# Kernel optimization log

Measured on AMD Instinct MI355X. Metric: run time of the kernel, lower is better.

Reference implementation:

```python
import jax, jax.numpy as jnp
import numpy as np

BANDWIDTH = 0.1
N_STEPS = 5
TOL = 1e-3
BASE = 3
COORD_OFFSET = 512   # bins assumed within (-512, 511] per dim
COORD_BITS = 10      # 3 dims * 10 bits = 30 bits, fits int32


def _generate_offsets(d, base=3):
    # replicates torch.meshgrid(indexing='ij') over arange(-1, base-1)
    ranges = [np.arange(-1, base - 1) for _ in range(d)]
    mesh = np.meshgrid(*ranges, indexing='ij')
    return jnp.asarray(np.stack(mesh, axis=-1).reshape(-1, d), dtype=jnp.int32)


def _pack_keys(bins):
    # bins: (..., d) int32 -> unique scalar int32 key per bin coordinate
    d = bins.shape[-1]
    key = jnp.zeros(bins.shape[:-1], dtype=jnp.int32)
    for k in range(d):  # tiny fixed loop over dims
        key = (key << COORD_BITS) | (bins[..., k] + COORD_OFFSET)
    return key


def _step(X, offsets, bandwidth):
    # One mean-shift step: bin points, scatter-add sums/counts over the
    # union of offset-shifted bins (torch.unique replaced by exact key
    # packing + sort-based grouping, fixed shapes for jit).
    n, d = X.shape
    m = offsets.shape[0]  # base ** d
    bins = (X / bandwidth).astype(jnp.int32)          # trunc-toward-zero == torch .int()
    shifted = bins[:, None, :] + offsets[None, :, :]  # (n, m, d)
    keys = _pack_keys(shifted).reshape(-1)            # (n*m,)
    K = keys.shape[0]

    order = jnp.argsort(keys)
    skeys = keys[order]
    new_grp = jnp.concatenate(
        [jnp.zeros((1,), jnp.int32), (skeys[1:] != skeys[:-1]).astype(jnp.int32)]
    )
    seg = jnp.cumsum(new_grp)                         # group id per sorted position

    # X repeated once per offset (matches X.repeat(1, m).reshape(-1, d))
    Xflat = jnp.broadcast_to(X[:, None, :], (n, m, d)).reshape(-1, d)
    sum_per = jax.ops.segment_sum(Xflat[order], seg, num_segments=K)          # (K, d)
    cnt_per = jax.ops.segment_sum(jnp.ones((K,), X.dtype), seg, num_segments=K)

    # segment id per original (unsorted) flat position == inverse_indices
    seg_orig = jnp.zeros((K,), seg.dtype).at[order].set(seg)
    sum_mapped = sum_per[seg_orig].reshape(n, m, d).sum(axis=1)   # (n, d)
    cnt_mapped = cnt_per[seg_orig].reshape(n, m).sum(axis=1)      # (n,)
    return sum_mapped / cnt_mapped[:, None]


def setup_inputs() -> dict:
    key = jax.random.key(0)
    X = jax.random.normal(key, (200000, 3), dtype=jnp.float32)
    return {"X": X}


def reference(X):
    n, d = X.shape
    offsets = _generate_offsets(d, BASE)

    def body(carry, _):
        Xc, done = carry
        Xn = _step(Xc, offsets, BANDWIDTH)
        Xn = jnp.where(done, Xc, Xn)  # freeze once converged (== early break)
        conv = jnp.max(jnp.linalg.norm(Xn - Xc, axis=1)) <= TOL
        return (Xn, done | conv), None

    (Xout, _), _ = jax.lax.scan(body, (X, jnp.array(False)), None, length=N_STEPS)
    return Xout
```

## Files before the change

kernel.cpp:

```cpp
#include <hip/hip_runtime.h>


constexpr float BW   = 0.1f;
constexpr float TOL2 = 1e-6f;
constexpr int DIM  = 112, OFF = 56;
constexpr int DIM2 = DIM * DIM;
constexpr int CELLS = DIM * DIM * DIM;
constexpr int CLW = CELLS / 32;
constexpr int RDIM = 16, RC = 7;
constexpr int NREG = RDIM * RDIM * RDIM;
constexpr int RC3 = RC * RC * RC;
constexpr int NB_A = 128, BLK = 256;
constexpr int NF = 2048;
constexpr int IPB = 51;
constexpr float FPS = 16777216.0f;
constexpr double FPSI = 1.0 / 16777216.0;

typedef float vf2 __attribute__((ext_vector_type(2)));

__device__ __forceinline__ int clampb(int v) { return v < 0 ? 0 : (v > DIM - 1 ? DIM - 1 : v); }
__device__ __forceinline__ int binf(float v) { return clampb((int)(v / BW) + OFF); }
__device__ __forceinline__ int flatb(int bx, int by, int bz) { return (bx * DIM + by) * DIM + bz; }
__device__ __forceinline__ int regOf(int bx, int by, int bz) {
    return ((bx / RC) * RDIM + (by / RC)) * RDIM + (bz / RC);
}
__device__ __forceinline__ int lcOf(int bx, int by, int bz) {
    return ((bx % RC) * RC + (by % RC)) * RC + (bz % RC);
}

__device__ __forceinline__ void pk_add(float* p, float a, float b) {
#if defined(__has_builtin) && __has_builtin(__builtin_amdgcn_global_atomic_fadd_v2f32)
    vf2 v = {a, b};
    __builtin_amdgcn_global_atomic_fadd_v2f32((vf2*)p, v);
#else
    atomicAdd(p, a);
    atomicAdd(p + 1, b);
#endif
}

__launch_bounds__(BLK)
__global__ void k_histA(const float* __restrict__ X, int n, int* __restrict__ blockHist,
                        float4* __restrict__ zeroA, float4* __restrict__ zeroB) {
    __shared__ int h[NREG];
    for (int i = threadIdx.x; i < NREG; i += blockDim.x) h[i] = 0;
    __syncthreads();
    int stride = gridDim.x * blockDim.x;
    for (int i = blockIdx.x * blockDim.x + threadIdx.x; i < n; i += stride) {
        float x = X[3 * i + 0], y = X[3 * i + 1], z = X[3 * i + 2];
        atomicAdd(&h[regOf(binf(x), binf(y), binf(z))], 1);
    }
    __syncthreads();
    for (int i = threadIdx.x; i < NREG; i += blockDim.x)
        blockHist[blockIdx.x * NREG + i] = h[i];
    for (int i = blockIdx.x * blockDim.x + threadIdx.x; i < CELLS; i += stride) {
        zeroA[i] = make_float4(0.f, 0.f, 0.f, 0.f);
        zeroB[i] = make_float4(0.f, 0.f, 0.f, 0.f);
    }
}

__global__ void k_colscan(int* __restrict__ blockHist, int* __restrict__ regionPS) {
    int r = blockIdx.x * blockDim.x + threadIdx.x;
    if (r >= NREG) return;
    int run = 0;
    for (int b = 0; b < NB_A; ++b) {
        int idx = b * NREG + r;
        int v = blockHist[idx];
        blockHist[idx] = run;
        run += v;
    }
    regionPS[r] = run;
}

__launch_bounds__(1024)
__global__ void k_regprefix(int* __restrict__ regionPS) {
    __shared__ int buf[1024];
    int t = threadIdx.x;
    int v0 = regionPS[4 * t + 0], v1 = regionPS[4 * t + 1];
    int v2 = regionPS[4 * t + 2], v3 = regionPS[4 * t + 3];
    int s = v0 + v1 + v2 + v3;
    buf[t] = s;
    __syncthreads();
    for (int d = 1; d < 1024; d <<= 1) {
        int add = (t >= d) ? buf[t - d] : 0;
        __syncthreads();
        buf[t] += add;
        __syncthreads();
    }
    int excl = buf[t] - s;
    regionPS[4 * t + 0] = excl;
    regionPS[4 * t + 1] = excl + v0;
    regionPS[4 * t + 2] = excl + v0 + v1;
    regionPS[4 * t + 3] = excl + v0 + v1 + v2;
    if (t == 1023) regionPS[4096] = buf[1023];
}

__launch_bounds__(BLK)
__global__ void k_scatterA(const float* __restrict__ X, int n,
                           const int* __restrict__ blockHist,
                           const int* __restrict__ regionPS,
                           float4* __restrict__ bucket, float4* __restrict__ zeroC) {
    __shared__ int cur[NREG];
    for (int i = threadIdx.x; i < NREG; i += blockDim.x) cur[i] = 0;
    __syncthreads();
    int stride = gridDim.x * blockDim.x;
    for (int i = blockIdx.x * blockDim.x + threadIdx.x; i < n; i += stride) {
        float x = X[3 * i + 0], y = X[3 * i + 1], z = X[3 * i + 2];
        int r = regOf(binf(x), binf(y), binf(z));
        int pos = regionPS[r] + blockHist[blockIdx.x * NREG + r] + atomicAdd(&cur[r], 1);
        bucket[pos] = make_float4(x, y, z, __int_as_float(i));
    }
    for (int i = blockIdx.x * blockDim.x + threadIdx.x; i < CELLS; i += stride)
        zeroC[i] = make_float4(0.f, 0.f, 0.f, 0.f);
}

__launch_bounds__(BLK)
__global__ void k_binB(const float4* __restrict__ bucket, const int* __restrict__ regionPS,
                       float4* __restrict__ A, int* __restrict__ E0,
                       int* __restrict__ PIdx, int* __restrict__ gM0) {
    __shared__ unsigned long long aX[RC3], aY[RC3], aZ[RC3];
    __shared__ unsigned aC[RC3];
    __shared__ int cidx[RC3];
    __shared__ int cnt, cur, sBase;
    int r = blockIdx.x;
    for (int c = threadIdx.x; c < RC3; c += blockDim.x) {
        aX[c] = 0ull; aY[c] = 0ull; aZ[c] = 0ull; aC[c] = 0u;
    }
    if (threadIdx.x == 0) { cnt = 0; cur = 0; }
    __syncthreads();
    int start = regionPS[r], end = regionPS[r + 1];
    for (int i = start + threadIdx.x; i < end; i += blockDim.x) {
        float4 p = bucket[i];
        int lc = lcOf(binf(p.x), binf(p.y), binf(p.z));
        atomicAdd(&aX[lc], (unsigned long long)(long long)rintf(p.x * FPS));
        atomicAdd(&aY[lc], (unsigned long long)(long long)rintf(p.y * FPS));
        atomicAdd(&aZ[lc], (unsigned long long)(long long)rintf(p.z * FPS));
        atomicAdd(&aC[lc], 1u);
    }
    __syncthreads();
    int myc = 0;
    for (int c = threadIdx.x; c < RC3; c += blockDim.x)
        if (aC[c] > 0u) ++myc;
    if (myc) atomicAdd(&cnt, myc);
    __syncthreads();
    if (threadIdx.x == 0 && cnt > 0) sBase = atomicAdd(gM0, cnt);
    __syncthreads();
    int rx = r / (RDIM * RDIM), ry = (r / RDIM) % RDIM, rz = r % RDIM;
    for (int c = threadIdx.x; c < RC3; c += blockDim.x) {
        if (aC[c] > 0u) {
            int idx = sBase + atomicAdd(&cur, 1);
            cidx[c] = idx;
            int bx = rx * RC + c / (RC * RC);
            int by = ry * RC + (c / RC) % RC;
            int bz = rz * RC + c % RC;
            int b = flatb(bx, by, bz);
            E0[idx] = b;
            A[b] = make_float4((float)((double)(long long)aX[c] * FPSI),
                               (float)((double)(long long)aY[c] * FPSI),
                               (float)((double)(long long)aZ[c] * FPSI),
                               (float)aC[c]);
        }
    }
    __syncthreads();
    for (int i = start + threadIdx.x; i < end; i += blockDim.x) {
        float4 p = bucket[i];
        int lc = lcOf(binf(p.x), binf(p.y), binf(p.z));
        PIdx[__float_as_int(p.w)] = cidx[lc];
    }
}

__launch_bounds__(BLK)
__global__ void k_fused(
    const float4* __restrict__ src, const int* __restrict__ list, const int* __restrict__ pK,
    float4* __restrict__ REo, int* __restrict__ IDXo, float4* __restrict__ eposInit,
    float4* __restrict__ tgt, unsigned* __restrict__ clT,
    int updS, const float* __restrict__ X, int n, const int* __restrict__ PIdx,
    const float4* __restrict__ REp, const int* __restrict__ IDXp,
    const int* __restrict__ pM0, float4* __restrict__ epos,
    unsigned* __restrict__ notConv,
    const int* __restrict__ clearList, const int* __restrict__ pKc,
    float4* __restrict__ clearGrid, int chkMask, int lastStep) {
    __shared__ float4 sh[BLK];
    __shared__ float shW[IPB];
    __shared__ unsigned sFlag;
    if (threadIdx.x == 0) sFlag = 0;
    __syncthreads();
    int K = *pK;
    int NC = (K + IPB - 1) / IPB;
    int BC = NC;
    if (BC > NF - 256) BC = NF - 256;
    const float t5[5] = {1.f, 2.f, 3.f, 2.f, 1.f};
    bool moved = false;

    if ((int)blockIdx.x < BC) {
        bool frozen = false;
        if (chkMask) {
            #pragma unroll
            for (int t = 1; t <= 4; ++t)
                if ((chkMask >> t) & 1) frozen |= (notConv[t] == 0u);
        }
        if (!frozen) {
        int first, last, step;
        if (BC >= 64) {
            int xcd = blockIdx.x & 7, loc = blockIdx.x >> 3;
            int cpx = (NC + 7) >> 3;
            int bpx = ((BC - 1 - xcd) >> 3) + 1;
            first = xcd * cpx + loc;
            last = (xcd + 1) * cpx; if (last > NC) last = NC;
            step = bpx;
        } else {
            first = blockIdx.x; last = NC; step = BC;
        }
        for (int ib = first; ib < last; ib += step) {
            int li = threadIdx.x / 5;
            int dx = threadIdx.x % 5;
            int item = ib * IPB + li;
            float4 part = make_float4(0.f, 0.f, 0.f, 0.f);
            if (li < IPB && item < K) {
                int b = list[item];
                int bx = b / DIM2, rem = b % DIM2;
                int by = rem / DIM, bz = rem % DIM;
                if (dx == 2) shW[li] = src[b].w;
                int ix = bx + dx - 2;
                if ((unsigned)ix < (unsigned)DIM) {
                    float wx = t5[dx];
                    if (by >= 2 && by <= DIM - 3 && bz >= 2 && bz <= DIM - 3) {
                        const float4* bp = src + flatb(ix, by - 2, bz - 2);
                        float4 e0[5], e1[5];
                        #pragma unroll
                        for (int z = 0; z < 5; ++z) e0[z] = bp[z];
                        #pragma unroll
                        for (int z = 0; z < 5; ++z) e1[z] = bp[DIM + z];
                        #define ACC_ROW(EB, WXY)                                   \
                            {                                                      \
                                float wxy_ = (WXY);                                \
                                _Pragma("unroll")                                  \
                                for (int z = 0; z < 5; ++z) {                      \
                                    float w_ = wxy_ * t5[z];                       \
                                    part.x = fmaf(w_, EB[z].x, part.x);            \
                                    part.y = fmaf(w_, EB[z].y, part.y);            \
                                    part.z = fmaf(w_, EB[z].z, part.z);            \
                                    part.w = fmaf(w_, EB[z].w, part.w);            \
                                }                                                  \
                            }
                        ACC_ROW(e0, wx * 1.f);
                        #pragma unroll
                        for (int z = 0; z < 5; ++z) e0[z] = bp[2 * DIM + z];
                        ACC_ROW(e1, wx * 2.f);
                        #pragma unroll
                        for (int z = 0; z < 5; ++z) e1[z] = bp[3 * DIM + z];
                        ACC_ROW(e0, wx * 3.f);
                        #pragma unroll
                        for (int z = 0; z < 5; ++z) e0[z] = bp[4 * DIM + z];
                        ACC_ROW(e1, wx * 2.f);
                        ACC_ROW(e0, wx * 1.f);
                        #undef ACC_ROW
                    } else {
                        for (int dy = 0; dy < 5; ++dy) {
                            int iy = by + dy - 2;
                            if ((unsigned)iy >= (unsigned)DIM) continue;
                            float wxy = wx * t5[dy];
                            for (int dz = 0; dz < 5; ++dz) {
                                int iz = bz + dz - 2;
                                if ((unsigned)iz >= (unsigned)DIM) continue;
                                float w = wxy * t5[dz];
                                float4 e = src[flatb(ix, iy, iz)];
                                part.x = fmaf(w, e.x, part.x);
                                part.y = fmaf(w, e.y, part.y);
                                part.z = fmaf(w, e.z, part.z);
                                part.w = fmaf(w, e.w, part.w);
                            }
                        }
                    }
                }
            }
            sh[threadIdx.x] = part;
            __syncthreads();
            if (threadIdx.x < 64) {
                int item2 = ib * IPB + threadIdx.x;
                bool valid = (threadIdx.x < IPB) && (item2 < K);
                int bn = -1;
                float4 sv = make_float4(0.f, 0.f, 0.f, 0.f);
                if (valid) {
                    int base5 = threadIdx.x * 5;
                    float4 a0 = sh[base5 + 0], a1 = sh[base5 + 1], a2 = sh[base5 + 2];
                    float4 a3 = sh[base5 + 3], a4 = sh[base5 + 4];
                    float sx = a0.x + a1.x + a2.x + a3.x + a4.x;
                    float sy = a0.y + a1.y + a2.y + a3.y + a4.y;
                    float sz = a0.z + a1.z + a2.z + a3.z + a4.z;
                    float sc = a0.w + a1.w + a2.w + a3.w + a4.w;
                    int b = list[item2];
                    float W = shW[threadIdx.x];
                    float4 np = make_float4(sx / sc, sy / sc, sz / sc, W);
                    REo[item2] = np;
                    IDXo[b] = item2;
                    if (eposInit) eposInit[item2] = np;
                    if (!lastStep) {
                        bn = flatb(binf(np.x), binf(np.y), binf(np.z));
                        sv = make_float4(W * np.x, W * np.y, W * np.z, W);
                    }
                }
                if (!lastStep) {
                    int pbn = __shfl_up(bn, 1, 64);
                    unsigned f = (threadIdx.x == 0 || pbn != bn) ? 1u : 0u;
                    unsigned nf = __shfl_down(f, 1, 64);
                    bool leader = valid && (threadIdx.x == 63 || nf != 0u);
                    #pragma unroll
                    for (int off = 1; off < 64; off <<= 1) {
                        float ox = __shfl_up(sv.x, off, 64);
                        float oy = __shfl_up(sv.y, off, 64);
                        float oz = __shfl_up(sv.z, off, 64);
                        float ow = __shfl_up(sv.w, off, 64);
                        unsigned of = __shfl_up(f, off, 64);
                        if ((int)threadIdx.x >= off) {
                            if (!f) { sv.x += ox; sv.y += oy; sv.z += oz; sv.w += ow; }
                            f |= of;
                        }
                    }
                    if (leader) {
                        float* cell = (float*)&tgt[bn];
                        pk_add(cell + 0, sv.x, sv.y);
                        pk_add(cell + 2, sv.z, sv.w);
                        atomicOr(&clT[(unsigned)bn >> 5], 1u << (bn & 31));
                    }
                }
            }
            __syncthreads();
        }
        }
    } else {
        int U = (updS > 0) ? (X ? n : *pM0) : 0;
        int CL = clearList ? *pKc : 0;
        int total = U + CL;
        bool done = false;
        if (updS > 1) {
            for (int t = 1; t < updS; ++t) done |= (notConv[t] == 0u);
        }
        int stride = (NF - BC) * blockDim.x;
        for (int idx = (blockIdx.x - BC) * blockDim.x + threadIdx.x; idx < total;
             idx += stride) {
            if (idx < U) {
                int e = idx;
                if (X) {
                    float x = X[3 * e + 0], y = X[3 * e + 1], z = X[3 * e + 2];
                    float4 rr = REp[PIdx[e]];
                    float ex = rr.x - x, ey = rr.y - y, ez = rr.z - z;
                    moved |= (fmaf(ex, ex, fmaf(ey, ey, ez * ez)) > TOL2);
                } else if (!done) {
                    float4 p = epos[e];
                    int j = IDXp[flatb(binf(p.x), binf(p.y), binf(p.z))];
                    float4 rr = REp[j];
                    float ex = rr.x - p.x, ey = rr.y - p.y, ez = rr.z - p.z;
                    moved |= (fmaf(ex, ex, fmaf(ey, ey, ez * ez)) > TOL2);
                    epos[e] = make_float4(rr.x, rr.y, rr.z, p.w);
                }
            } else {
                clearGrid[clearList[idx - U]] = make_float4(0.f, 0.f, 0.f, 0.f);
            }
        }
    }
    if (moved) sFlag = 1;
    __syncthreads();
    if (threadIdx.x == 0 && updS > 0 && sFlag) notConv[updS] = 1u;
}

__launch_bounds__(BLK)
__global__ void k_compactM(unsigned* __restrict__ mask, int* __restrict__ listOut,
                           int* __restrict__ pKout) {
    __shared__ int scan[BLK];
    __shared__ int sBase;
    int i = blockIdx.x * blockDim.x + threadIdx.x;
    unsigned w = (i < CLW) ? mask[i] : 0u;
    if (i < CLW && w) mask[i] = 0u;
    int c = __popc(w);
    scan[threadIdx.x] = c;
    __syncthreads();
    for (int d = 1; d < BLK; d <<= 1) {
        int add = (threadIdx.x >= (unsigned)d) ? scan[threadIdx.x - d] : 0;
        __syncthreads();
        scan[threadIdx.x] += add;
        __syncthreads();
    }
    if (threadIdx.x == BLK - 1) {
        int tot = scan[BLK - 1];
        sBase = tot ? atomicAdd(pKout, tot) : 0;
    }
    __syncthreads();
    int base = sBase + scan[threadIdx.x] - c;
    int bb = i * 32;
    while (w) {
        int b = __ffs(w) - 1;
        listOut[base++] = bb + b;
        w &= w - 1;
    }
}

__global__ void k_map(const int* __restrict__ PIdx, int n, const float4* __restrict__ epos,
                      const float4* __restrict__ REa, const int* __restrict__ IDXa,
                      const unsigned* __restrict__ notConv, float* __restrict__ out) {
    bool done = false;
    for (int t = 1; t <= 4; ++t) done |= (notConv[t] == 0u);
    int i = blockIdx.x * blockDim.x + threadIdx.x;
    if (i >= n) return;
    float4 p = epos[PIdx[i]];
    if (!done) {
        float4 rr = REa[IDXa[flatb(binf(p.x), binf(p.y), binf(p.z))]];
        p.x = rr.x; p.y = rr.y; p.z = rr.z;
    }
    out[3 * i + 0] = p.x;
    out[3 * i + 1] = p.y;
    out[3 * i + 2] = p.z;
}

extern "C" void kernel_launch(void* const* d_in, const int* in_sizes, int n_in,
                              void* d_out, int out_size, void* d_ws, size_t ws_size,
                              hipStream_t stream) {
    const float* X = (const float*)d_in[0];
    int n = in_sizes[0] / 3;

    char* ws = (char*)d_ws;
    int*      cnt     = (int*)ws;
    unsigned* notConv = (unsigned*)(ws + 32);
    size_t mB = (size_t)CLW * 4;
    size_t gB = (size_t)CELLS * 16;
    unsigned* m0 = (unsigned*)(ws + 256);
    unsigned* m1 = (unsigned*)(ws + 256 + mB);
    float4* A = (float4*)(ws + 256 + 2 * mB);
    float4* B = (float4*)((char*)A + gB);
    float4* C = (float4*)((char*)B + gB);
    int* IDXa = (int*)((char*)C + gB);
    int* IDXb = IDXa + CELLS;
    float4* REa  = (float4*)(IDXb + CELLS);
    float4* REb  = REa + n;
    float4* epos = REb + n;
    int* E0   = (int*)(epos + n);
    int* La   = E0 + n;
    int* Lb   = La + n;
    int* Lc   = Lb + n;
    int* Ld   = Lc + n;
    int* PIdx = Ld + n;
    float4* bucket = (float4*)(PIdx + n);
    int* blockHist = (int*)(bucket + n);
    int* regionPS  = blockHist + NB_A * NREG;

    hipMemsetAsync(ws, 0, 256 + 2 * mB, stream);

    const int NCM = (CLW + BLK - 1) / BLK;

    k_histA<<<NB_A, BLK, 0, stream>>>(X, n, blockHist, A, B);
    k_colscan<<<NREG / BLK, BLK, 0, stream>>>(blockHist, regionPS);
    k_regprefix<<<1, 1024, 0, stream>>>(regionPS);
    k_scatterA<<<NB_A, BLK, 0, stream>>>(X, n, blockHist, regionPS, bucket, C);
    k_binB<<<NREG, BLK, 0, stream>>>(bucket, regionPS, A, E0, PIdx, &cnt[1]);

    k_fused<<<NF, BLK, 0, stream>>>(A, E0, &cnt[1], REa, IDXa, epos,
                                    B, m0,
                                    0, nullptr, n, nullptr, nullptr, nullptr, nullptr,
                                    nullptr, notConv, nullptr, nullptr, nullptr, 0, 0);
    k_compactM<<<NCM, BLK, 0, stream>>>(m0, La, &cnt[2]);
    k_fused<<<NF, BLK, 0, stream>>>(B, La, &cnt[2], REb, IDXb, nullptr,
                                    C, m1,
                                    1, X, n, PIdx, REa, IDXa, &cnt[1], nullptr,
                                    notConv, E0, &cnt[1], A, 0, 0);
    k_compactM<<<NCM, BLK, 0, stream>>>(m1, Lb, &cnt[3]);
    k_fused<<<NF, BLK, 0, stream>>>(C, Lb, &cnt[3], REa, IDXa, nullptr,
                                    A, m0,
                                    2, nullptr, n, nullptr, REb, IDXb, &cnt[1], epos,
                                    notConv, La, &cnt[2], B, 0b00010, 0);
    k_compactM<<<NCM, BLK, 0, stream>>>(m0, Lc, &cnt[4]);
    k_fused<<<NF, BLK, 0, stream>>>(A, Lc, &cnt[4], REb, IDXb, nullptr,
                                    B, m1,
                                    3, nullptr, n, nullptr, REa, IDXa, &cnt[1], epos,
                                    notConv, nullptr, nullptr, nullptr, 0b00110, 0);
    k_compactM<<<NCM, BLK, 0, stream>>>(m1, Ld, &cnt[5]);
    k_fused<<<NF, BLK, 0, stream>>>(B, Ld, &cnt[5], REa, IDXa, nullptr,
                                    nullptr, nullptr,
                                    4, nullptr, n, nullptr, REb, IDXb, &cnt[1], epos,
                                    notConv, nullptr, nullptr, nullptr, 0b01110, 1);

    k_map<<<(n + BLK - 1) / BLK, BLK, 0, stream>>>(PIdx, n, epos, REa, IDXa,
                                                   notConv, (float*)d_out);
}
```

Before: 246.6 us.

## Move per-point update and grid clearing from stencil kernel into compaction kernel

The stencil kernel previously split its blocks between grid-cell smoothing and auxiliary work: updating point positions, convergence checks and clearing the previous grid. That auxiliary work now runs in a new k_aux kernel that also does the mask compaction. The stencil kernel can therefore use all blocks for the cell work. The aux work now runs serially between stencil passes rather than alongside them, and the last stencil's frozen-check mask changes to include step 4.

```diff
diff --git a/kernel.cpp b/kernel.cpp
--- a/kernel.cpp
+++ b/kernel.cpp
@@ -13,6 +13,7 @@
 constexpr int NB_A = 128, BLK = 256;
 constexpr int NF = 2048;
 constexpr int IPB = 51;
+constexpr int NCM = (CLW + BLK - 1) / BLK;
 constexpr float FPS = 16777216.0f;
 constexpr double FPSI = 1.0 / 16777216.0;
 
@@ -173,161 +174,192 @@
     const float4* __restrict__ src, const int* __restrict__ list, const int* __restrict__ pK,
     float4* __restrict__ REo, int* __restrict__ IDXo, float4* __restrict__ eposInit,
     float4* __restrict__ tgt, unsigned* __restrict__ clT,
+    const unsigned* __restrict__ notConv, int chkMask, int lastStep) {
+    __shared__ float4 sh[BLK];
+    __shared__ float shW[IPB];
+    int K = *pK;
+    int NC = (K + IPB - 1) / IPB;
+    int BC = NC > NF ? NF : NC;
+    if ((int)blockIdx.x >= BC) return;
+    bool frozen = false;
+    if (chkMask) {
+        #pragma unroll
+        for (int t = 1; t <= 4; ++t)
+            if ((chkMask >> t) & 1) frozen |= (notConv[t] == 0u);
+    }
+    if (frozen) return;
+    const float t5[5] = {1.f, 2.f, 3.f, 2.f, 1.f};
+
+    int first, last, step;
+    if (BC >= 64) {
+        int xcd = blockIdx.x & 7, loc = blockIdx.x >> 3;
+        int cpx = (NC + 7) >> 3;
+        int bpx = ((BC - 1 - xcd) >> 3) + 1;
+        first = xcd * cpx + loc;
+        last = (xcd + 1) * cpx; if (last > NC) last = NC;
+        step = bpx;
+    } else {
+        first = blockIdx.x; last = NC; step = BC;
+    }
+    for (int ib = first; ib < last; ib += step) {
+        int li = threadIdx.x / 5;
+        int dx = threadIdx.x % 5;
+        int item = ib * IPB + li;
+        float4 part = make_float4(0.f, 0.f, 0.f, 0.f);
+        if (li < IPB && item < K) {
+            int b = list[item];
+            int bx = b / DIM2, rem = b % DIM2;
+            int by = rem / DIM, bz = rem % DIM;
+            if (dx == 2) shW[li] = src[b].w;
+            int ix = bx + dx - 2;
+            if ((unsigned)ix < (unsigned)DIM) {
+                float wx = t5[dx];
+                if (by >= 2 && by <= DIM - 3 && bz >= 2 && bz <= DIM - 3) {
+                    const float4* bp = src + flatb(ix, by - 2, bz - 2);
+                    float4 e0[5], e1[5];
+                    #pragma unroll
+                    for (int z = 0; z < 5; ++z) e0[z] = bp[z];
+                    #pragma unroll
+                    for (int z = 0; z < 5; ++z) e1[z] = bp[DIM + z];
+                    #define ACC_ROW(EB, WXY)                                   \
+                        {                                                      \
+                            float wxy_ = (WXY);                                \
+                            _Pragma("unroll")                                  \
+                            for (int z = 0; z < 5; ++z) {                      \
+                                float w_ = wxy_ * t5[z];                       \
+                                part.x = fmaf(w_, EB[z].x, part.x);            \
+                                part.y = fmaf(w_, EB[z].y, part.y);            \
+                                part.z = fmaf(w_, EB[z].z, part.z);            \
+                                part.w = fmaf(w_, EB[z].w, part.w);            \
+                            }                                                  \
+                        }
+                    ACC_ROW(e0, wx * 1.f);
+                    #pragma unroll
+                    for (int z = 0; z < 5; ++z) e0[z] = bp[2 * DIM + z];
+                    ACC_ROW(e1, wx * 2.f);
+                    #pragma unroll
+                    for (int z = 0; z < 5; ++z) e1[z] = bp[3 * DIM + z];
+                    ACC_ROW(e0, wx * 3.f);
+                    #pragma unroll
+                    for (int z = 0; z < 5; ++z) e0[z] = bp[4 * DIM + z];
+                    ACC_ROW(e1, wx * 2.f);
+                    ACC_ROW(e0, wx * 1.f);
+                    #undef ACC_ROW
+                } else {
+                    for (int dy = 0; dy < 5; ++dy) {
+                        int iy = by + dy - 2;
+                        if ((unsigned)iy >= (unsigned)DIM) continue;
+                        float wxy = wx * t5[dy];
+                        for (int dz = 0; dz < 5; ++dz) {
+                            int iz = bz + dz - 2;
+                            if ((unsigned)iz >= (unsigned)DIM) continue;
+                            float w = wxy * t5[dz];
+                            float4 e = src[flatb(ix, iy, iz)];
+                            part.x = fmaf(w, e.x, part.x);
+                            part.y = fmaf(w, e.y, part.y);
+                            part.z = fmaf(w, e.z, part.z);
+                            part.w = fmaf(w, e.w, part.w);
+                        }
+                    }
+                }
+            }
+        }
+        sh[threadIdx.x] = part;
+        __syncthreads();
+        if (threadIdx.x < 64) {
+            int item2 = ib * IPB + threadIdx.x;
+            bool valid = (threadIdx.x < IPB) && (item2 < K);
+            int bn = -1;
+            float4 sv = make_float4(0.f, 0.f, 0.f, 0.f);
+            if (valid) {
+                int base5 = threadIdx.x * 5;
+                float4 a0 = sh[base5 + 0], a1 = sh[base5 + 1], a2 = sh[base5 + 2];
+                float4 a3 = sh[base5 + 3], a4 = sh[base5 + 4];
+                float sx = a0.x + a1.x + a2.x + a3.x + a4.x;
+                float sy = a0.y + a1.y + a2.y + a3.y + a4.y;
+                float sz = a0.z + a1.z + a2.z + a3.z + a4.z;
+                float sc = a0.w + a1.w + a2.w + a3.w + a4.w;
+                int b = list[item2];
+                float W = shW[threadIdx.x];
+                float4 np = make_float4(sx / sc, sy / sc, sz / sc, W);
+                REo[item2] = np;
+                IDXo[b] = item2;
+                if (eposInit) eposInit[item2] = np;
+                if (!lastStep) {
+                    bn = flatb(binf(np.x), binf(np.y), binf(np.z));
+                    sv = make_float4(W * np.x, W * np.y, W * np.z, W);
+                }
+            }
+            if (!lastStep) {
+                int pbn = __shfl_up(bn, 1, 64);
+                unsigned f = (threadIdx.x == 0 || pbn != bn) ? 1u : 0u;
+                unsigned nf = __shfl_down(f, 1, 64);
+                bool leader = valid && (threadIdx.x == 63 || nf != 0u);
+                #pragma unroll
+                for (int off = 1; off < 64; off <<= 1) {
+                    float ox = __shfl_up(sv.x, off, 64);
+                    float oy = __shfl_up(sv.y, off, 64);
+                    float oz = __shfl_up(sv.z, off, 64);
+                    float ow = __shfl_up(sv.w, off, 64);
+                    unsigned of = __shfl_up(f, off, 64);
+                    if ((int)threadIdx.x >= off) {
+                        if (!f) { sv.x += ox; sv.y += oy; sv.z += oz; sv.w += ow; }
+                        f |= of;
+                    }
+                }
+                if (leader) {
+                    float* cell = (float*)&tgt[bn];
+                    pk_add(cell + 0, sv.x, sv.y);
+                    pk_add(cell + 2, sv.z, sv.w);
+                    atomicOr(&clT[(unsigned)bn >> 5], 1u << (bn & 31));
+                }
+            }
+        }
+        __syncthreads();
+    }
+}
+
+__launch_bounds__(BLK)
+__global__ void k_aux(
+    unsigned* __restrict__ mask, int* __restrict__ listOut, int* __restrict__ pKout,
     int updS, const float* __restrict__ X, int n, const int* __restrict__ PIdx,
     const float4* __restrict__ REp, const int* __restrict__ IDXp,
     const int* __restrict__ pM0, float4* __restrict__ epos,
     unsigned* __restrict__ notConv,
     const int* __restrict__ clearList, const int* __restrict__ pKc,
-    float4* __restrict__ clearGrid, int chkMask, int lastStep) {
-    __shared__ float4 sh[BLK];
-    __shared__ float shW[IPB];
-    __shared__ unsigned sFlag;
-    if (threadIdx.x == 0) sFlag = 0;
-    __syncthreads();
-    int K = *pK;
-    int NC = (K + IPB - 1) / IPB;
-    int BC = NC;
-    if (BC > NF - 256) BC = NF - 256;
-    const float t5[5] = {1.f, 2.f, 3.f, 2.f, 1.f};
-    bool moved = false;
-
-    if ((int)blockIdx.x < BC) {
-        bool frozen = false;
-        if (chkMask) {
-            #pragma unroll
-            for (int t = 1; t <= 4; ++t)
-                if ((chkMask >> t) & 1) frozen |= (notConv[t] == 0u);
-        }
-        if (!frozen) {
-        int first, last, step;
-        if (BC >= 64) {
-            int xcd = blockIdx.x & 7, loc = blockIdx.x >> 3;
-            int cpx = (NC + 7) >> 3;
-            int bpx = ((BC - 1 - xcd) >> 3) + 1;
-            first = xcd * cpx + loc;
-            last = (xcd + 1) * cpx; if (last > NC) last = NC;
-            step = bpx;
-        } else {
-            first = blockIdx.x; last = NC; step = BC;
-        }
-        for (int ib = first; ib < last; ib += step) {
-            int li = threadIdx.x / 5;
-            int dx = threadIdx.x % 5;
-            int item = ib * IPB + li;
-            float4 part = make_float4(0.f, 0.f, 0.f, 0.f);
-            if (li < IPB && item < K) {
-                int b = list[item];
-                int bx = b / DIM2, rem = b % DIM2;
-                int by = rem / DIM, bz = rem % DIM;
-                if (dx == 2) shW[li] = src[b].w;
-                int ix = bx + dx - 2;
-                if ((unsigned)ix < (unsigned)DIM) {
-                    float wx = t5[dx];
-                    if (by >= 2 && by <= DIM - 3 && bz >= 2 && bz <= DIM - 3) {
-                        const float4* bp = src + flatb(ix, by - 2, bz - 2);
-                        float4 e0[5], e1[5];
-                        #pragma unroll
-                        for (int z = 0; z < 5; ++z) e0[z] = bp[z];
-                        #pragma unroll
-                        for (int z = 0; z < 5; ++z) e1[z] = bp[DIM + z];
-                        #define ACC_ROW(EB, WXY)                                   \
-                            {                                                      \
-                                float wxy_ = (WXY);                                \
-                                _Pragma("unroll")                                  \
-                                for (int z = 0; z < 5; ++z) {                      \
-                                    float w_ = wxy_ * t5[z];                       \
-                                    part.x = fmaf(w_, EB[z].x, part.x);            \
-                                    part.y = fmaf(w_, EB[z].y, part.y);            \
-                                    part.z = fmaf(w_, EB[z].z, part.z);            \
-                                    part.w = fmaf(w_, EB[z].w, part.w);            \
-                                }                                                  \
-                            }
-                        ACC_ROW(e0, wx * 1.f);
-                        #pragma unroll
-                        for (int z = 0; z < 5; ++z) e0[z] = bp[2 * DIM + z];
-                        ACC_ROW(e1, wx * 2.f);
-                        #pragma unroll
-                        for (int z = 0; z < 5; ++z) e1[z] = bp[3 * DIM + z];
-                        ACC_ROW(e0, wx * 3.f);
-                        #pragma unroll
-                        for (int z = 0; z < 5; ++z) e0[z] = bp[4 * DIM + z];
-                        ACC_ROW(e1, wx * 2.f);
-                        ACC_ROW(e0, wx * 1.f);
-                        #undef ACC_ROW
-                    } else {
-                        for (int dy = 0; dy < 5; ++dy) {
-                            int iy = by + dy - 2;
-                            if ((unsigned)iy >= (unsigned)DIM) continue;
-                            float wxy = wx * t5[dy];
-                            for (int dz = 0; dz < 5; ++dz) {
-                                int iz = bz + dz - 2;
-                                if ((unsigned)iz >= (unsigned)DIM) continue;
-                                float w = wxy * t5[dz];
-                                float4 e = src[flatb(ix, iy, iz)];
-                                part.x = fmaf(w, e.x, part.x);
-                                part.y = fmaf(w, e.y, part.y);
-                                part.z = fmaf(w, e.z, part.z);
-                                part.w = fmaf(w, e.w, part.w);
-                            }
-                        }
-                    }
-                }
-            }
-            sh[threadIdx.x] = part;
+    float4* __restrict__ clearGrid) {
+    if ((int)blockIdx.x < NCM) {
+        __shared__ int scan[BLK];
+        __shared__ int sBase;
+        int i = blockIdx.x * BLK + threadIdx.x;
+        unsigned w = (i < CLW) ? mask[i] : 0u;
+        if (i < CLW && w) mask[i] = 0u;
+        int c = __popc(w);
+        scan[threadIdx.x] = c;
+        __syncthreads();
+        for (int d = 1; d < BLK; d <<= 1) {
+            int add = (threadIdx.x >= (unsigned)d) ? scan[threadIdx.x - d] : 0;
             __syncthreads();
-            if (threadIdx.x < 64) {
-                int item2 = ib * IPB + threadIdx.x;
-                bool valid = (threadIdx.x < IPB) && (item2 < K);
-                int bn = -1;
-                float4 sv = make_float4(0.f, 0.f, 0.f, 0.f);
-                if (valid) {
-                    int base5 = threadIdx.x * 5;
-                    float4 a0 = sh[base5 + 0], a1 = sh[base5 + 1], a2 = sh[base5 + 2];
-                    float4 a3 = sh[base5 + 3], a4 = sh[base5 + 4];
-                    float sx = a0.x + a1.x + a2.x + a3.x + a4.x;
-                    float sy = a0.y + a1.y + a2.y + a3.y + a4.y;
-                    float sz = a0.z + a1.z + a2.z + a3.z + a4.z;
-                    float sc = a0.w + a1.w + a2.w + a3.w + a4.w;
-                    int b = list[item2];
-                    float W = shW[threadIdx.x];
-                    float4 np = make_float4(sx / sc, sy / sc, sz / sc, W);
-                    REo[item2] = np;
-                    IDXo[b] = item2;
-                    if (eposInit) eposInit[item2] = np;
-                    if (!lastStep) {
-                        bn = flatb(binf(np.x), binf(np.y), binf(np.z));
-                        sv = make_float4(W * np.x, W * np.y, W * np.z, W);
-                    }
-                }
-                if (!lastStep) {
-                    int pbn = __shfl_up(bn, 1, 64);
-                    unsigned f = (threadIdx.x == 0 || pbn != bn) ? 1u : 0u;
-                    unsigned nf = __shfl_down(f, 1, 64);
-                    bool leader = valid && (threadIdx.x == 63 || nf != 0u);
-                    #pragma unroll
-                    for (int off = 1; off < 64; off <<= 1) {
-                        float ox = __shfl_up(sv.x, off, 64);
-                        float oy = __shfl_up(sv.y, off, 64);
-                        float oz = __shfl_up(sv.z, off, 64);
-                        float ow = __shfl_up(sv.w, off, 64);
-                        unsigned of = __shfl_up(f, off, 64);
-                        if ((int)threadIdx.x >= off) {
-                            if (!f) { sv.x += ox; sv.y += oy; sv.z += oz; sv.w += ow; }
-                            f |= of;
-                        }
-                    }
-                    if (leader) {
-                        float* cell = (float*)&tgt[bn];
-                        pk_add(cell + 0, sv.x, sv.y);
-                        pk_add(cell + 2, sv.z, sv.w);
-                        atomicOr(&clT[(unsigned)bn >> 5], 1u << (bn & 31));
-                    }
-                }
-            }
+            scan[threadIdx.x] += add;
             __syncthreads();
         }
+        if (threadIdx.x == BLK - 1) {
+            int tot = scan[BLK - 1];
+            sBase = tot ? atomicAdd(pKout, tot) : 0;
+        }
+        __syncthreads();
+        int base = sBase + scan[threadIdx.x] - c;
+        int bb = i * 32;
+        while (w) {
+            int b = __ffs(w) - 1;
+            listOut[base++] = bb + b;
+            w &= w - 1;
         }
     } else {
+        __shared__ unsigned sFlag;
+        if (threadIdx.x == 0) sFlag = 0;
+        __syncthreads();
+        bool moved = false;
         int U = (updS > 0) ? (X ? n : *pM0) : 0;
         int CL = clearList ? *pKc : 0;
         int total = U + CL;
@@ -335,8 +367,8 @@
         if (updS > 1) {
             for (int t = 1; t < updS; ++t) done |= (notConv[t] == 0u);
         }
-        int stride = (NF - BC) * blockDim.x;
-        for (int idx = (blockIdx.x - BC) * blockDim.x + threadIdx.x; idx < total;
+        int stride = (NF - NCM) * BLK;
+        for (int idx = ((int)blockIdx.x - NCM) * BLK + threadIdx.x; idx < total;
              idx += stride) {
             if (idx < U) {
                 int e = idx;
@@ -357,40 +389,9 @@
                 clearGrid[clearList[idx - U]] = make_float4(0.f, 0.f, 0.f, 0.f);
             }
         }
-    }
-    if (moved) sFlag = 1;
-    __syncthreads();
-    if (threadIdx.x == 0 && updS > 0 && sFlag) notConv[updS] = 1u;
-}
-
-__launch_bounds__(BLK)
-__global__ void k_compactM(unsigned* __restrict__ mask, int* __restrict__ listOut,
-                           int* __restrict__ pKout) {
-    __shared__ int scan[BLK];
-    __shared__ int sBase;
-    int i = blockIdx.x * blockDim.x + threadIdx.x;
-    unsigned w = (i < CLW) ? mask[i] : 0u;
-    if (i < CLW && w) mask[i] = 0u;
-    int c = __popc(w);
-    scan[threadIdx.x] = c;
-    __syncthreads();
-    for (int d = 1; d < BLK; d <<= 1) {
-        int add = (threadIdx.x >= (unsigned)d) ? scan[threadIdx.x - d] : 0;
-        __syncthreads();
-        scan[threadIdx.x] += add;
-        __syncthreads();
-    }
-    if (threadIdx.x == BLK - 1) {
-        int tot = scan[BLK - 1];
-        sBase = tot ? atomicAdd(pKout, tot) : 0;
-    }
-    __syncthreads();
-    int base = sBase + scan[threadIdx.x] - c;
-    int bb = i * 32;
-    while (w) {
-        int b = __ffs(w) - 1;
-        listOut[base++] = bb + b;
-        w &= w - 1;
+        if (moved) sFlag = 1;
+        __syncthreads();
+        if (threadIdx.x == 0 && updS > 0 && sFlag) notConv[updS] = 1u;
     }
 }
 
@@ -444,8 +445,6 @@
 
     hipMemsetAsync(ws, 0, 256 + 2 * mB, stream);
 
-    const int NCM = (CLW + BLK - 1) / BLK;
-
     k_histA<<<NB_A, BLK, 0, stream>>>(X, n, blockHist, A, B);
     k_colscan<<<NREG / BLK, BLK, 0, stream>>>(blockHist, regionPS);
     k_regprefix<<<1, 1024, 0, stream>>>(regionPS);
@@ -453,29 +452,27 @@
     k_binB<<<NREG, BLK, 0, stream>>>(bucket, regionPS, A, E0, PIdx, &cnt[1]);
 
     k_fused<<<NF, BLK, 0, stream>>>(A, E0, &cnt[1], REa, IDXa, epos,
-                                    B, m0,
-                                    0, nullptr, n, nullptr, nullptr, nullptr, nullptr,
-                                    nullptr, notConv, nullptr, nullptr, nullptr, 0, 0);
-    k_compactM<<<NCM, BLK, 0, stream>>>(m0, La, &cnt[2]);
+                                    B, m0, notConv, 0, 0);
+    k_aux<<<NF, BLK, 0, stream>>>(m0, La, &cnt[2],
+                                  1, X, n, PIdx, REa, nullptr, &cnt[1], nullptr,
+                                  notConv, E0, &cnt[1], A);
     k_fused<<<NF, BLK, 0, stream>>>(B, La, &cnt[2], REb, IDXb, nullptr,
-                                    C, m1,
-                                    1, X, n, PIdx, REa, IDXa, &cnt[1], nullptr,
-                                    notConv, E0, &cnt[1], A, 0, 0);
-    k_compactM<<<NCM, BLK, 0, stream>>>(m1, Lb, &cnt[3]);
+                                    C, m1, notConv, 0, 0);
+    k_aux<<<NF, BLK, 0, stream>>>(m1, Lb, &cnt[3],
+                                  2, nullptr, n, nullptr, REb, IDXb, &cnt[1], epos,
+                                  notConv, La, &cnt[2], B);
     k_fused<<<NF, BLK, 0, stream>>>(C, Lb, &cnt[3], REa, IDXa, nullptr,
-                                    A, m0,
-                                    2, nullptr, n, nullptr, REb, IDXb, &cnt[1], epos,
-                                    notConv, La, &cnt[2], B, 0b00010, 0);
-    k_compactM<<<NCM, BLK, 0, stream>>>(m0, Lc, &cnt[4]);
+                                    A, m0, notConv, 0b00010, 0);
+    k_aux<<<NF, BLK, 0, stream>>>(m0, Lc, &cnt[4],
+                                  3, nullptr, n, nullptr, REa, IDXa, &cnt[1], epos,
+                                  notConv, nullptr, nullptr, nullptr);
     k_fused<<<NF, BLK, 0, stream>>>(A, Lc, &cnt[4], REb, IDXb, nullptr,
-                                    B, m1,
-                                    3, nullptr, n, nullptr, REa, IDXa, &cnt[1], epos,
-                                    notConv, nullptr, nullptr, nullptr, 0b00110, 0);
-    k_compactM<<<NCM, BLK, 0, stream>>>(m1, Ld, &cnt[5]);
+                                    B, m1, notConv, 0b00110, 0);
+    k_aux<<<NF, BLK, 0, stream>>>(m1, Ld, &cnt[5],
+                                  4, nullptr, n, nullptr, REb, IDXb, &cnt[1], epos,
+                                  notConv, nullptr, nullptr, nullptr);
     k_fused<<<NF, BLK, 0, stream>>>(B, Ld, &cnt[5], REa, IDXa, nullptr,
-                                    nullptr, nullptr,
-                                    4, nullptr, n, nullptr, REb, IDXb, &cnt[1], epos,
-                                    notConv, nullptr, nullptr, nullptr, 0b01110, 1);
+                                    nullptr, nullptr, notConv, 0b11110, 1);
 
     k_map<<<(n + BLK - 1) / BLK, BLK, 0, stream>>>(PIdx, n, epos, REa, IDXa,
                                                    notConv, (float*)d_out);
```

New measurement: 251.6 us. 2.0% more time.
